# Performance work log

Hardware: AMD Instinct MI355X
Metric: run time of the kernel (lower is better)

Reference implementation:

```python
import jax, jax.numpy as jnp
import numpy as np

B, N_MAX, C = 8, 8192, 384
G, K, H = 512, 32, 6
DH = C // H


def setup_inputs() -> dict:
    key = jax.random.key(0)
    ks = jax.random.split(key, 7)
    upscaled_feats = jax.random.normal(ks[0], (B, N_MAX, C), dtype=jnp.float32)
    grouping_idx = jax.random.randint(ks[1], (B, G, K), 0, N_MAX, dtype=jnp.int64)
    mask = (jax.random.uniform(ks[2], (B, G, K)) < 0.9).astype(jnp.float32)
    grouping_point_mask = mask.at[:, :, 0].set(1.0)
    # Attention params (qkv_bias=False), proj with bias, LayerScale gamma
    s = 1.0 / np.sqrt(C)
    w_qkv = jax.random.normal(ks[3], (3 * C, C), dtype=jnp.float32) * s
    w_proj = jax.random.normal(ks[4], (C, C), dtype=jnp.float32) * s
    b_proj = jnp.zeros((C,), dtype=jnp.float32)
    gamma = jnp.full((C,), 1e-5, dtype=jnp.float32)
    return {
        "upscaled_feats": upscaled_feats,
        "grouping_idx": grouping_idx,
        "grouping_point_mask": grouping_point_mask,
        "w_qkv": w_qkv,
        "w_proj": w_proj,
        "b_proj": b_proj,
        "gamma": gamma,
    }


def reference(upscaled_feats, grouping_idx, grouping_point_mask, w_qkv, w_proj, b_proj, gamma):
    Bv, Nmax, Cd = upscaled_feats.shape
    _, Gn, Kn = grouping_idx.shape
    # fill_empty_indices: -1 -> 0 (contributions zeroed by the mask later)
    idx = jnp.where(grouping_idx < 0, 0, grouping_idx).astype(jnp.int32)
    # masked_gather: [B, G, K, C]
    x_groups = jnp.take_along_axis(
        upscaled_feats[:, None, :, :], idx[..., None], axis=2)
    xg = x_groups.reshape(Bv * Gn, Kn, Cd)
    key_mask = grouping_point_mask.reshape(Bv * Gn, Kn)  # 1 = valid key

    # --- multi-head self attention within each group ---
    qkv = jnp.einsum('bnc,dc->bnd', xg, w_qkv)  # [BG, K, 3C]
    qkv = qkv.reshape(Bv * Gn, Kn, 3, H, DH)
    q = qkv[:, :, 0].transpose(0, 2, 1, 3)  # [BG, H, K, Dh]
    k = qkv[:, :, 1].transpose(0, 2, 1, 3)
    v = qkv[:, :, 2].transpose(0, 2, 1, 3)
    scale = DH ** -0.5
    scores = jnp.einsum('bhqd,bhkd->bhqk', q, k) * scale
    bias = jnp.where(key_mask > 0, 0.0, -1e9)[:, None, None, :]  # mask keys
    attn = jax.nn.softmax(scores + bias, axis=-1)  # [BG, H, K, K]
    out = jnp.einsum('bhqk,bhkd->bhqd', attn, v)
    out = out.transpose(0, 2, 1, 3).reshape(Bv * Gn, Kn, Cd)
    out = jnp.einsum('bnc,dc->bnd', out, w_proj) + b_proj
    x_groups_attn = out.reshape(Bv, Gn, Kn, Cd)

    # --- scatter-add average back onto points ---
    src = (x_groups_attn * grouping_point_mask[..., None]).reshape(-1, Cd)
    seg = (idx.astype(jnp.int32) + (jnp.arange(Bv, dtype=jnp.int32) * Nmax)[:, None, None]).reshape(-1)
    acc = jax.ops.segment_sum(src, seg, num_segments=Bv * Nmax).reshape(Bv, Nmax, Cd)
    cnt = jax.ops.segment_sum(grouping_point_mask.reshape(-1), seg,
                              num_segments=Bv * Nmax).reshape(Bv, Nmax, 1)
    averaged = acc / jnp.clip(cnt, 1.0)

    return upscaled_feats + averaged * gamma
```

## Files before the change

### kernel.cpp

```cpp
#include <hip/hip_runtime.h>
#include <hip/hip_bf16.h>

#define B_   8
#define NMAX 8192
#define C_   384
#define G_   512
#define K_   32
#define H_   6
#define DH_  64
#define CAP_ 16

typedef short bvec8 __attribute__((ext_vector_type(8)));
typedef short bvec4 __attribute__((ext_vector_type(4)));
typedef _Float16 hvec4 __attribute__((ext_vector_type(4)));
typedef float f32x4 __attribute__((ext_vector_type(4)));
typedef unsigned int u32x4 __attribute__((ext_vector_type(4)));

__device__ __forceinline__ short f2bf(float f) {
    union { __hip_bfloat16 b; short s; } u;
    u.b = __float2bfloat16(f);
    return u.s;
}

__device__ __forceinline__ int swzA(int row, int colb) { return row * 768 + (colb ^ ((row & 7) << 4)); }
__device__ __forceinline__ int swzS(int row, int colb) { return row * 384 + (colb ^ ((row & 7) << 4)); }

__global__ void convw_kernel(const float* __restrict__ wqkv, const float* __restrict__ wproj,
                             short* __restrict__ wq_frag, short* __restrict__ wp_frag) {
    int i = blockIdx.x * 256 + threadIdx.x;
    if (i < 55296) {
        int lane = i & 63, t = i >> 6;
        int nt = t & 3, kk = (t >> 2) % 12, hh = (t >> 2) / 12;
        int row  = hh * 64 + nt * 16 + (lane & 15);
        int col0 = kk * 32 + (lane >> 4) * 8;
        const float* src = wqkv + (size_t)row * C_ + col0;
        bvec8 v;
        #pragma unroll
        for (int e = 0; e < 8; ++e) v[e] = f2bf(src[e]);
        *(bvec8*)(wq_frag + (size_t)i * 8) = v;
    } else if (i < 55296 + 18432) {
        int j = i - 55296;
        int lane = j & 63, t = j >> 6;
        int nt = t & 3, kk = (t >> 2) % 12, h = (t >> 2) / 12;
        int row  = h * 64 + nt * 16 + (lane & 15);
        int col0 = kk * 32 + (lane >> 4) * 8;
        const float* src = wproj + (size_t)row * C_ + col0;
        bvec8 v;
        #pragma unroll
        for (int e = 0; e < 8; ++e) v[e] = f2bf(src[e]);
        *(bvec8*)(wp_frag + (size_t)j * 8) = v;
    }
}

__global__ void fill_kernel(const int* __restrict__ gidx, const float* __restrict__ gmask,
                            int* __restrict__ fillcnt, unsigned short* __restrict__ list) {
    int t = blockIdx.x * 256 + threadIdx.x;
    if (t >= B_ * G_ * K_) return;
    float m = gmask[t];
    if (m <= 0.f) return;
    int v = gidx[t];
    v = v < 0 ? 0 : v;
    int b = t >> 14;
    int bn = b * NMAX + v;
    int pos = atomicAdd(&fillcnt[bn], 1);
    if (pos < CAP_) list[(size_t)bn * CAP_ + pos] = (unsigned short)(t - (b << 14));
}

#define QKV_M     128
#define QKV_STAGE (QKV_M * 768)
#define QKV_LDS   (QKV_M * 768 + QKV_M * 384)
__global__ __launch_bounds__(768, 3) void qkv_kernel(
    const float* __restrict__ feats, const short* __restrict__ wq_frag,
    unsigned char* __restrict__ qb, unsigned char* __restrict__ kb,
    unsigned char* __restrict__ vb) {
    extern __shared__ char sm[];
    char* stage = sm + QKV_STAGE;
    const int tid  = threadIdx.x;
    const int lane = tid & 63;
    const int h2   = tid >> 6;
    const int h    = h2 >> 1;
    const int mh   = h2 & 1;
    const int l15  = lane & 15;
    const int l4   = lane >> 4;
    const int pt0  = blockIdx.x * QKV_M;

    #pragma unroll
    for (int i = 0; i < 16; ++i) {
        int p = i * 768 + tid;
        int row = p / 96, seg = p % 96;
        f32x4 f = *(const f32x4*)(feats + (size_t)(pt0 + row) * C_ + seg * 4);
        bvec4 v4 = { f2bf(f[0]), f2bf(f[1]), f2bf(f[2]), f2bf(f[3]) };
        *(bvec4*)(sm + swzA(row, seg * 8)) = v4;
    }
    __syncthreads();

    for (int mat = 0; mat < 3; ++mat) {
        const short* wb = wq_frag + (size_t)((mat * 6 + h) * 48) * 512;
        unsigned char* dst = (mat == 0) ? qb : (mat == 1) ? kb : vb;
        f32x4 acc[2][8];
        #pragma unroll
        for (int mt = 0; mt < 2; ++mt)
            #pragma unroll
            for (int nt = 0; nt < 8; ++nt) acc[mt][nt] = (f32x4){0.f, 0.f, 0.f, 0.f};
        #pragma unroll
        for (int kk = 0; kk < 12; ++kk) {
            bvec8 xb[8];
            #pragma unroll
            for (int nt = 0; nt < 8; ++nt)
                xb[nt] = *(const bvec8*)(sm + swzA(nt * 16 + l15, kk * 64 + l4 * 16));
            #pragma unroll
            for (int mt = 0; mt < 2; ++mt) {
                bvec8 wf = *(const bvec8*)(wb + (size_t)((kk * 4 + mh * 2 + mt) * 64 + lane) * 8);
                #pragma unroll
                for (int nt = 0; nt < 8; ++nt)
                    acc[mt][nt] = __builtin_amdgcn_mfma_f32_16x16x32_bf16(wf, xb[nt], acc[mt][nt], 0, 0, 0);
            }
        }
        #pragma unroll
        for (int mt = 0; mt < 2; ++mt)
            #pragma unroll
            for (int nt = 0; nt < 8; ++nt) {
                int w = __builtin_amdgcn_cvt_pk_fp8_f32(acc[mt][nt][0], acc[mt][nt][1], 0, false);
                w = __builtin_amdgcn_cvt_pk_fp8_f32(acc[mt][nt][2], acc[mt][nt][3], w, true);
                *(unsigned int*)(stage + swzS(nt * 16 + l15, h * DH_ + mh * 32 + mt * 16 + l4 * 4))
                    = (unsigned int)w;
            }
        __syncthreads();
        #pragma unroll
        for (int it = 0; it < 4; ++it) {
            int chunk = it * 768 + tid;
            int row = chunk / 24, off = chunk % 24;
            u32x4 v = *(const u32x4*)(stage + swzS(row, off * 16));
            *(u32x4*)(dst + (size_t)(pt0 + row) * C_ + off * 16) = v;
        }
        __syncthreads();
    }
}

#define AQ_OFF   0
#define AK_OFF   13824
#define AV_OFF   27648
#define AMASK    40704
#define AIDX     40832
#define ATTN_LDS 40960

template<bool SLOT>
__global__ __launch_bounds__(384, 5) void attn2_kernel(
    const int* __restrict__ gidx, const float* __restrict__ gmask,
    const unsigned char* __restrict__ qb, const unsigned char* __restrict__ kb,
    const unsigned char* __restrict__ vb,
    unsigned char* __restrict__ slotbuf, float* __restrict__ acc_out) {
    extern __shared__ char sm[];
    float* mask_lds = (float*)(sm + AMASK);
    int*   idx_lds  = (int*)(sm + AIDX);

    const int tid  = threadIdx.x;
    const int lane = tid & 63;
    const int h    = tid >> 6;
    const int bg   = blockIdx.x;
    const int b    = bg >> 9;
    const int l15  = lane & 15;
    const int l4   = lane >> 4;

    if (tid < 32) {
        int v = gidx[(size_t)bg * K_ + tid];
        v = v < 0 ? 0 : v;
        idx_lds[tid]  = v;
        mask_lds[tid] = gmask[(size_t)bg * K_ + tid];
    }
    __syncthreads();

    char* qh = sm + AQ_OFF + h * 2304;
    char* kh = sm + AK_OFF + h * 2304;
    char* vh = sm + AV_OFF + h * 2176;

    const int t8 = lane >> 3, c8 = lane & 7;
    #pragma unroll
    for (int i = 0; i < 4; ++i) {
        int t = i * 8 + t8;
        size_t base = (size_t)(b * NMAX + idx_lds[t]) * C_ + h * DH_;
        long qv = *(const long*)(qb + base + c8 * 8);
        long kv = *(const long*)(kb + base + c8 * 8);
        long vv = *(const long*)(vb + base + c8 * 8);
        *(long*)(qh + t * 72 + c8 * 8) = qv;
        *(long*)(kh + t * 72 + c8 * 8) = kv;
        *(int*)(vh + t * 68 + c8 * 8)     = (int)(vv & 0xffffffffL);
        *(int*)(vh + t * 68 + c8 * 8 + 4) = (int)(((unsigned long)vv) >> 32);
    }

    f32x4 sc[2][2];
    #pragma unroll
    for (int mt = 0; mt < 2; ++mt)
        #pragma unroll
        for (int nt = 0; nt < 2; ++nt) sc[mt][nt] = (f32x4){0.f, 0.f, 0.f, 0.f};
    #pragma unroll
    for (int kk = 0; kk < 2; ++kk) {
        long ka0 = *(const long*)(kh + l15 * 72 + kk * 32 + l4 * 8);
        long ka1 = *(const long*)(kh + (16 + l15) * 72 + kk * 32 + l4 * 8);
        long qa0 = *(const long*)(qh + l15 * 72 + kk * 32 + l4 * 8);
        long qa1 = *(const long*)(qh + (16 + l15) * 72 + kk * 32 + l4 * 8);
        sc[0][0] = __builtin_amdgcn_mfma_f32_16x16x32_fp8_fp8(ka0, qa0, sc[0][0], 0, 0, 0);
        sc[0][1] = __builtin_amdgcn_mfma_f32_16x16x32_fp8_fp8(ka0, qa1, sc[0][1], 0, 0, 0);
        sc[1][0] = __builtin_amdgcn_mfma_f32_16x16x32_fp8_fp8(ka1, qa0, sc[1][0], 0, 0, 0);
        sc[1][1] = __builtin_amdgcn_mfma_f32_16x16x32_fp8_fp8(ka1, qa1, sc[1][1], 0, 0, 0);
    }

    float bk[2][4];
    #pragma unroll
    for (int mt = 0; mt < 2; ++mt)
        #pragma unroll
        for (int j = 0; j < 4; ++j)
            bk[mt][j] = mask_lds[mt * 16 + l4 * 4 + j] > 0.f ? 0.f : -1e30f;

    hvec4 pfrag[2][2];
    #pragma unroll
    for (int nt = 0; nt < 2; ++nt) {
        float s[2][4];
        float mx = -1e30f;
        #pragma unroll
        for (int mt = 0; mt < 2; ++mt)
            #pragma unroll
            for (int j = 0; j < 4; ++j) {
                s[mt][j] = sc[mt][nt][j] * 0.125f + bk[mt][j];
                mx = fmaxf(mx, s[mt][j]);
            }
        mx = fmaxf(mx, __shfl_xor(mx, 16));
        mx = fmaxf(mx, __shfl_xor(mx, 32));
        float sum = 0.f;
        #pragma unroll
        for (int mt = 0; mt < 2; ++mt)
            #pragma unroll
            for (int j = 0; j < 4; ++j) {
                s[mt][j] = __expf(s[mt][j] - mx);
                sum += s[mt][j];
            }
        sum += __shfl_xor(sum, 16);
        sum += __shfl_xor(sum, 32);
        float inv = 1.f / sum;
        #pragma unroll
        for (int mt = 0; mt < 2; ++mt)
            pfrag[mt][nt] = (hvec4){ (_Float16)(s[mt][0] * inv), (_Float16)(s[mt][1] * inv),
                                     (_Float16)(s[mt][2] * inv), (_Float16)(s[mt][3] * inv) };
    }

    hvec4 vfrag[2][4];
    #pragma unroll
    for (int c = 0; c < 2; ++c)
        #pragma unroll
        for (int dt = 0; dt < 4; ++dt) {
            hvec4 vv;
            #pragma unroll
            for (int e = 0; e < 4; ++e) {
                int byt = *(const unsigned char*)(vh + (c * 16 + l4 * 4 + e) * 68 + dt * 16 + l15);
                vv[e] = (_Float16)__builtin_amdgcn_cvt_f32_fp8(byt, 0);
            }
            vfrag[c][dt] = vv;
        }

    f32x4 po[4][2];
    #pragma unroll
    for (int dt = 0; dt < 4; ++dt)
        #pragma unroll
        for (int qt = 0; qt < 2; ++qt) po[dt][qt] = (f32x4){0.f, 0.f, 0.f, 0.f};
    #pragma unroll
    for (int c = 0; c < 2; ++c)
        #pragma unroll
        for (int dt = 0; dt < 4; ++dt)
            #pragma unroll
            for (int qt = 0; qt < 2; ++qt)
                po[dt][qt] = __builtin_amdgcn_mfma_f32_16x16x16f16(vfrag[c][dt], pfrag[c][qt], po[dt][qt], 0, 0, 0);

    if constexpr (SLOT) {
        __syncthreads();
        char* stage = sm + AQ_OFF;
        #pragma unroll
        for (int dt = 0; dt < 4; ++dt)
            #pragma unroll
            for (int qt = 0; qt < 2; ++qt) {
                int w = __builtin_amdgcn_cvt_pk_fp8_f32(po[dt][qt][0], po[dt][qt][1], 0, false);
                w = __builtin_amdgcn_cvt_pk_fp8_f32(po[dt][qt][2], po[dt][qt][3], w, true);
                *(unsigned int*)(stage + swzS(qt * 16 + l15, h * DH_ + dt * 16 + l4 * 4))
                    = (unsigned int)w;
            }
        __syncthreads();
        #pragma unroll
        for (int it = 0; it < 2; ++it) {
            int chunk = it * 384 + tid;
            int row = chunk / 24, off = chunk % 24;
            u32x4 v = *(const u32x4*)(stage + swzS(row, off * 16));
            *(u32x4*)(slotbuf + ((size_t)bg * K_ + row) * C_ + off * 16) = v;
        }
    } else {
        #pragma unroll
        for (int qt = 0; qt < 2; ++qt) {
            int tok = qt * 16 + l15;
            float mk = mask_lds[tok];
            size_t rowb = (size_t)(b * NMAX + idx_lds[tok]) * C_ + h * DH_ + l4 * 4;
            #pragma unroll
            for (int dt = 0; dt < 4; ++dt)
                #pragma unroll
                for (int j = 0; j < 4; ++j)
                    if (mk > 0.f) atomicAdd(acc_out + rowb + dt * 16 + j, po[dt][qt][j]);
        }
    }
}

#define AP2_LDS (32 * 768)
__global__ __launch_bounds__(384, 5) void avgproj2_kernel(
    const float* __restrict__ feats, const int* __restrict__ fillcnt,
    const unsigned short* __restrict__ list, const unsigned char* __restrict__ slotbuf,
    const short* __restrict__ wp_frag, const float* __restrict__ bproj,
    const float* __restrict__ gamma, float* __restrict__ out) {
    extern __shared__ char sm[];
    const int tid  = threadIdx.x;
    const int lane = tid & 63;
    const int h    = tid >> 6;
    const int l15  = lane & 15;
    const int l4   = lane >> 4;
    const int p0   = blockIdx.x * 32;

    {
        int p = tid / 12, part = tid % 12;
        int bn = p0 + p;
        int b  = bn >> 13;
        int c  = fillcnt[bn];
        int cc = c < CAP_ ? c : CAP_;
        f32x4 s[8];
        #pragma unroll
        for (int u = 0; u < 8; ++u) s[u] = (f32x4){0.f, 0.f, 0.f, 0.f};
        for (int e = 0; e < cc; ++e) {
            int sl = list[(size_t)bn * CAP_ + e];
            const unsigned char* row = slotbuf + ((size_t)(b << 14) + sl) * C_ + part * 32;
            u32x4 w0 = *(const u32x4*)row;
            u32x4 w1 = *(const u32x4*)(row + 16);
            #pragma unroll
            for (int q = 0; q < 4; ++q) {
                s[q][0] += __builtin_amdgcn_cvt_f32_fp8((int)w0[q], 0);
                s[q][1] += __builtin_amdgcn_cvt_f32_fp8((int)w0[q], 1);
                s[q][2] += __builtin_amdgcn_cvt_f32_fp8((int)w0[q], 2);
                s[q][3] += __builtin_amdgcn_cvt_f32_fp8((int)w0[q], 3);
                s[4 + q][0] += __builtin_amdgcn_cvt_f32_fp8((int)w1[q], 0);
                s[4 + q][1] += __builtin_amdgcn_cvt_f32_fp8((int)w1[q], 1);
                s[4 + q][2] += __builtin_amdgcn_cvt_f32_fp8((int)w1[q], 2);
                s[4 + q][3] += __builtin_amdgcn_cvt_f32_fp8((int)w1[q], 3);
            }
        }
        float inv = 1.f / (float)(c < 1 ? 1 : c);
        #pragma unroll
        for (int u = 0; u < 8; ++u) {
            bvec4 w = { f2bf(s[u][0] * inv), f2bf(s[u][1] * inv),
                        f2bf(s[u][2] * inv), f2bf(s[u][3] * inv) };
            *(bvec4*)(sm + swzA(p, (part * 32 + u * 4) * 2)) = w;
        }
    }
    __syncthreads();

    f32x4 acc[4][2];
    #pragma unroll
    for (int mt = 0; mt < 4; ++mt)
        #pragma unroll
        for (int nt = 0; nt < 2; ++nt) acc[mt][nt] = (f32x4){0.f, 0.f, 0.f, 0.f};
    const short* wb = wp_frag + (size_t)(h * 48) * 512;
    #pragma unroll
    for (int kk = 0; kk < 12; ++kk) {
        bvec8 xb[2];
        #pragma unroll
        for (int nt = 0; nt < 2; ++nt)
            xb[nt] = *(const bvec8*)(sm + swzA(nt * 16 + l15, kk * 64 + l4 * 16));
        #pragma unroll
        for (int mt = 0; mt < 4; ++mt) {
            bvec8 wf = *(const bvec8*)(wb + (size_t)((kk * 4 + mt) * 64 + lane) * 8);
            #pragma unroll
            for (int nt = 0; nt < 2; ++nt)
                acc[mt][nt] = __builtin_amdgcn_mfma_f32_16x16x32_bf16(wf, xb[nt], acc[mt][nt], 0, 0, 0);
        }
    }
    #pragma unroll
    for (int mt = 0; mt < 4; ++mt)
        #pragma unroll
        for (int nt = 0; nt < 2; ++nt) {
            int pt   = p0 + nt * 16 + l15;
            int col0 = h * DH_ + mt * 16 + l4 * 4;
            f32x4 fv = *(const f32x4*)(feats + (size_t)pt * C_ + col0);
            f32x4 gv = *(const f32x4*)(gamma + col0);
            f32x4 bv = *(const f32x4*)(bproj + col0);
            float has = fillcnt[pt] > 0 ? 1.f : 0.f;
            f32x4 r;
            #pragma unroll
            for (int j = 0; j < 4; ++j)
                r[j] = fv[j] + (acc[mt][nt][j] + bv[j]) * gv[j] * has;
            *(f32x4*)(out + (size_t)pt * C_ + col0) = r;
        }
}

#define AP_LDS (64 * 768)
__global__ __launch_bounds__(384, 4) void avgproj_kernel(
    const float* __restrict__ feats, const int* __restrict__ fillcnt,
    const short* __restrict__ wp_frag, const float* __restrict__ bproj,
    const float* __restrict__ gamma, float* out) {
    extern __shared__ char sm[];
    const int tid  = threadIdx.x;
    const int lane = tid & 63;
    const int h    = tid >> 6;
    const int l15  = lane & 15;
    const int l4   = lane >> 4;
    const int p0   = blockIdx.x * 64;

    {
        int p = tid / 6, part = tid - p * 6;
        int cv = fillcnt[p0 + p];
        float inv = 1.f / (float)(cv < 1 ? 1 : cv);
        const float* src = out + (size_t)(p0 + p) * C_ + part * 64;
        #pragma unroll
        for (int u = 0; u < 16; ++u) {
            f32x4 a = *(const f32x4*)(src + u * 4);
            bvec4 w = { f2bf(a[0] * inv), f2bf(a[1] * inv), f2bf(a[2] * inv), f2bf(a[3] * inv) };
            *(bvec4*)(sm + swzA(p, (part * 64 + u * 4) * 2)) = w;
        }
    }
    __syncthreads();

    f32x4 acc[4][4];
    #pragma unroll
    for (int mt = 0; mt < 4; ++mt)
        #pragma unroll
        for (int nt = 0; nt < 4; ++nt) acc[mt][nt] = (f32x4){0.f, 0.f, 0.f, 0.f};
    const short* wb = wp_frag + (size_t)(h * 48) * 512;
    #pragma unroll
    for (int kk = 0; kk < 12; ++kk) {
        bvec8 xb[4];
        #pragma unroll
        for (int nt = 0; nt < 4; ++nt)
            xb[nt] = *(const bvec8*)(sm + swzA(nt * 16 + l15, kk * 64 + l4 * 16));
        #pragma unroll
        for (int mt = 0; mt < 4; ++mt) {
            bvec8 wf = *(const bvec8*)(wb + (size_t)((kk * 4 + mt) * 64 + lane) * 8);
            #pragma unroll
            for (int nt = 0; nt < 4; ++nt)
                acc[mt][nt] = __builtin_amdgcn_mfma_f32_16x16x32_bf16(wf, xb[nt], acc[mt][nt], 0, 0, 0);
        }
    }
    #pragma unroll
    for (int mt = 0; mt < 4; ++mt)
        #pragma unroll
        for (int nt = 0; nt < 4; ++nt) {
            int pt   = p0 + nt * 16 + l15;
            int col0 = h * DH_ + mt * 16 + l4 * 4;
            f32x4 fv = *(const f32x4*)(feats + (size_t)pt * C_ + col0);
            f32x4 gv = *(const f32x4*)(gamma + col0);
            f32x4 bv = *(const f32x4*)(bproj + col0);
            float has = fillcnt[pt] > 0 ? 1.f : 0.f;
            f32x4 r;
            #pragma unroll
            for (int j = 0; j < 4; ++j)
                r[j] = fv[j] + (acc[mt][nt][j] + bv[j]) * gv[j] * has;
            *(f32x4*)(out + (size_t)pt * C_ + col0) = r;
        }
}

extern "C" void kernel_launch(void* const* d_in, const int* in_sizes, int n_in,
                              void* d_out, int out_size, void* d_ws, size_t ws_size,
                              hipStream_t stream) {
    const float* feats = (const float*)d_in[0];
    const int*   gidx  = (const int*)d_in[1];
    const float* gmask = (const float*)d_in[2];
    const float* wqkv  = (const float*)d_in[3];
    const float* wproj = (const float*)d_in[4];
    const float* bproj = (const float*)d_in[5];
    const float* gamma = (const float*)d_in[6];
    float* out = (float*)d_out;

    char* ws = (char*)d_ws;
    short* wq_frag = (short*)ws;
    short* wp_frag = (short*)(ws + 884736);
    int*   fillcnt = (int*)(ws + 1179648);
    unsigned short* list = (unsigned short*)(ws + 1441792);
    unsigned char* slotA = (unsigned char*)(ws + 3538944);
    unsigned char* qbA   = (unsigned char*)(ws + 53870592);
    unsigned char* kbA   = (unsigned char*)(ws + 79036416);
    unsigned char* vbA   = (unsigned char*)(ws + 104202240);
    const size_t neededA = 129368064;
    unsigned char* qbB = (unsigned char*)(ws + 1441792);
    unsigned char* kbB = (unsigned char*)(ws + 26607616);
    unsigned char* vbB = (unsigned char*)(ws + 51773440);

    convw_kernel<<<(55296 + 18432 + 255) / 256, 256, 0, stream>>>(wqkv, wproj, wq_frag, wp_frag);
    (void)hipMemsetAsync(fillcnt, 0, (size_t)B_ * NMAX * sizeof(int), stream);
    fill_kernel<<<(B_ * G_ * K_ + 255) / 256, 256, 0, stream>>>(gidx, gmask, fillcnt, list);

    if (ws_size >= neededA) {
        qkv_kernel<<<(B_ * NMAX) / QKV_M, 768, QKV_LDS, stream>>>(feats, wq_frag, qbA, kbA, vbA);
        attn2_kernel<true><<<B_ * G_, 384, ATTN_LDS, stream>>>(gidx, gmask, qbA, kbA, vbA,
                                                               slotA, nullptr);
        avgproj2_kernel<<<(B_ * NMAX) / 32, 384, AP2_LDS, stream>>>(feats, fillcnt, list, slotA,
                                                                    wp_frag, bproj, gamma, out);
    } else {
        (void)hipMemsetAsync(out, 0, (size_t)B_ * NMAX * C_ * sizeof(float), stream);
        qkv_kernel<<<(B_ * NMAX) / QKV_M, 768, QKV_LDS, stream>>>(feats, wq_frag, qbB, kbB, vbB);
        attn2_kernel<false><<<B_ * G_, 384, ATTN_LDS, stream>>>(gidx, gmask, qbB, kbB, vbB,
                                                                nullptr, out);
        avgproj_kernel<<<(B_ * NMAX) / 64, 384, AP_LDS, stream>>>(feats, fillcnt, wp_frag,
                                                                  bproj, gamma, out);
    }
}
```

Baseline: 197.4 us.

## Retile QKV MFMA to 4x4 and stage gather lists in LDS with unrolled loads

In the QKV projection kernel each wave now computes a 4x4 grid of MFMA tiles (64 output channels by 64 points) instead of 2x8. This cuts the LDS activation-fragment reads per k-step and adds more weight-fragment global loads. In the average/projection kernel, the block's slot lists are copied into LDS once and the gather loop is unrolled by two with nontemporal loads, so more fp8 row fetches are in flight. The extra 1 KB of LDS and a barrier could reduce occupancy slightly.

```diff
diff --git a/kernel.cpp b/kernel.cpp
--- a/kernel.cpp
+++ b/kernel.cpp
@@ -97,32 +97,32 @@
     for (int mat = 0; mat < 3; ++mat) {
         const short* wb = wq_frag + (size_t)((mat * 6 + h) * 48) * 512;
         unsigned char* dst = (mat == 0) ? qb : (mat == 1) ? kb : vb;
-        f32x4 acc[2][8];
-        #pragma unroll
-        for (int mt = 0; mt < 2; ++mt)
-            #pragma unroll
-            for (int nt = 0; nt < 8; ++nt) acc[mt][nt] = (f32x4){0.f, 0.f, 0.f, 0.f};
+        f32x4 acc[4][4];
+        #pragma unroll
+        for (int mt = 0; mt < 4; ++mt)
+            #pragma unroll
+            for (int nt = 0; nt < 4; ++nt) acc[mt][nt] = (f32x4){0.f, 0.f, 0.f, 0.f};
         #pragma unroll
         for (int kk = 0; kk < 12; ++kk) {
-            bvec8 xb[8];
-            #pragma unroll
-            for (int nt = 0; nt < 8; ++nt)
-                xb[nt] = *(const bvec8*)(sm + swzA(nt * 16 + l15, kk * 64 + l4 * 16));
-            #pragma unroll
-            for (int mt = 0; mt < 2; ++mt) {
-                bvec8 wf = *(const bvec8*)(wb + (size_t)((kk * 4 + mh * 2 + mt) * 64 + lane) * 8);
+            bvec8 xb[4];
+            #pragma unroll
+            for (int nt = 0; nt < 4; ++nt)
+                xb[nt] = *(const bvec8*)(sm + swzA(mh * 64 + nt * 16 + l15, kk * 64 + l4 * 16));
+            #pragma unroll
+            for (int mt = 0; mt < 4; ++mt) {
+                bvec8 wf = *(const bvec8*)(wb + (size_t)((kk * 4 + mt) * 64 + lane) * 8);
                 #pragma unroll
-                for (int nt = 0; nt < 8; ++nt)
+                for (int nt = 0; nt < 4; ++nt)
                     acc[mt][nt] = __builtin_amdgcn_mfma_f32_16x16x32_bf16(wf, xb[nt], acc[mt][nt], 0, 0, 0);
             }
         }
         #pragma unroll
-        for (int mt = 0; mt < 2; ++mt)
-            #pragma unroll
-            for (int nt = 0; nt < 8; ++nt) {
+        for (int mt = 0; mt < 4; ++mt)
+            #pragma unroll
+            for (int nt = 0; nt < 4; ++nt) {
                 int w = __builtin_amdgcn_cvt_pk_fp8_f32(acc[mt][nt][0], acc[mt][nt][1], 0, false);
                 w = __builtin_amdgcn_cvt_pk_fp8_f32(acc[mt][nt][2], acc[mt][nt][3], w, true);
-                *(unsigned int*)(stage + swzS(nt * 16 + l15, h * DH_ + mh * 32 + mt * 16 + l4 * 4))
+                *(unsigned int*)(stage + swzS(mh * 64 + nt * 16 + l15, h * DH_ + mt * 16 + l4 * 4))
                     = (unsigned int)w;
             }
         __syncthreads();
@@ -305,19 +305,25 @@
     }
 }
 
-#define AP2_LDS (32 * 768)
+#define AP2_LIST (32 * 768)
+#define AP2_LDS  (32 * 768 + 1024)
 __global__ __launch_bounds__(384, 5) void avgproj2_kernel(
     const float* __restrict__ feats, const int* __restrict__ fillcnt,
     const unsigned short* __restrict__ list, const unsigned char* __restrict__ slotbuf,
     const short* __restrict__ wp_frag, const float* __restrict__ bproj,
     const float* __restrict__ gamma, float* __restrict__ out) {
     extern __shared__ char sm[];
+    unsigned short* lds_list = (unsigned short*)(sm + AP2_LIST);
     const int tid  = threadIdx.x;
     const int lane = tid & 63;
     const int h    = tid >> 6;
     const int l15  = lane & 15;
     const int l4   = lane >> 4;
     const int p0   = blockIdx.x * 32;
+
+    if (tid < 256)
+        ((unsigned int*)lds_list)[tid] = ((const unsigned int*)(list + (size_t)p0 * CAP_))[tid];
+    __syncthreads();
 
     {
         int p = tid / 12, part = tid % 12;
@@ -328,11 +334,33 @@
         f32x4 s[8];
         #pragma unroll
         for (int u = 0; u < 8; ++u) s[u] = (f32x4){0.f, 0.f, 0.f, 0.f};
-        for (int e = 0; e < cc; ++e) {
-            int sl = list[(size_t)bn * CAP_ + e];
+        int e = 0;
+        for (; e + 1 < cc; e += 2) {
+            int sl0 = lds_list[p * CAP_ + e];
+            int sl1 = lds_list[p * CAP_ + e + 1];
+            const unsigned char* r0 = slotbuf + ((size_t)(b << 14) + sl0) * C_ + part * 32;
+            const unsigned char* r1 = slotbuf + ((size_t)(b << 14) + sl1) * C_ + part * 32;
+            u32x4 a0 = __builtin_nontemporal_load((const u32x4*)r0);
+            u32x4 a1 = __builtin_nontemporal_load((const u32x4*)(r0 + 16));
+            u32x4 b0 = __builtin_nontemporal_load((const u32x4*)r1);
+            u32x4 b1 = __builtin_nontemporal_load((const u32x4*)(r1 + 16));
+            #pragma unroll
+            for (int q = 0; q < 4; ++q) {
+                s[q][0] += __builtin_amdgcn_cvt_f32_fp8((int)a0[q], 0) + __builtin_amdgcn_cvt_f32_fp8((int)b0[q], 0);
+                s[q][1] += __builtin_amdgcn_cvt_f32_fp8((int)a0[q], 1) + __builtin_amdgcn_cvt_f32_fp8((int)b0[q], 1);
+                s[q][2] += __builtin_amdgcn_cvt_f32_fp8((int)a0[q], 2) + __builtin_amdgcn_cvt_f32_fp8((int)b0[q], 2);
+                s[q][3] += __builtin_amdgcn_cvt_f32_fp8((int)a0[q], 3) + __builtin_amdgcn_cvt_f32_fp8((int)b0[q], 3);
+                s[4 + q][0] += __builtin_amdgcn_cvt_f32_fp8((int)a1[q], 0) + __builtin_amdgcn_cvt_f32_fp8((int)b1[q], 0);
+                s[4 + q][1] += __builtin_amdgcn_cvt_f32_fp8((int)a1[q], 1) + __builtin_amdgcn_cvt_f32_fp8((int)b1[q], 1);
+                s[4 + q][2] += __builtin_amdgcn_cvt_f32_fp8((int)a1[q], 2) + __builtin_amdgcn_cvt_f32_fp8((int)b1[q], 2);
+                s[4 + q][3] += __builtin_amdgcn_cvt_f32_fp8((int)a1[q], 3) + __builtin_amdgcn_cvt_f32_fp8((int)b1[q], 3);
+            }
+        }
+        if (e < cc) {
+            int sl = lds_list[p * CAP_ + e];
             const unsigned char* row = slotbuf + ((size_t)(b << 14) + sl) * C_ + part * 32;
-            u32x4 w0 = *(const u32x4*)row;
-            u32x4 w1 = *(const u32x4*)(row + 16);
+            u32x4 w0 = __builtin_nontemporal_load((const u32x4*)row);
+            u32x4 w1 = __builtin_nontemporal_load((const u32x4*)(row + 16));
             #pragma unroll
             for (int q = 0; q < 4; ++q) {
                 s[q][0] += __builtin_amdgcn_cvt_f32_fp8((int)w0[q], 0);
```

Measured after the change: 194.7 us. No clear change (-1.4%).
